# Kernel tuning notes

Measured on AMD Instinct MI355X. Metric: run time of the kernel, lower is better.

## Reference

```python
import jax, jax.numpy as jnp
import numpy as np
import math

NUM_EMBED = 1024
EMBED_FEATS = 256
IN_FEATS = 512
COMMITMENT_COST = 0.25
B, T = 16, 4096


def setup_inputs() -> dict:
    key = jax.random.key(0)
    k1, k2, k3, k4 = jax.random.split(key, 4)
    inputs = jax.random.normal(k1, (B, IN_FEATS, T), dtype=jnp.float32)
    # Conv1d(kernel_size=1) == per-position linear: weight [E, C_in], bias [E]
    proj_w = jax.random.normal(k2, (EMBED_FEATS, IN_FEATS), dtype=jnp.float32) / np.sqrt(IN_FEATS)
    proj_b = jax.random.normal(k3, (EMBED_FEATS,), dtype=jnp.float32) * 0.01
    embed = jax.random.normal(k4, (NUM_EMBED, EMBED_FEATS), dtype=jnp.float32)
    return {"inputs": inputs, "proj_w": proj_w, "proj_b": proj_b, "embed": embed}


def reference(inputs, proj_w, proj_b, embed):
    sg = jax.lax.stop_gradient
    b, c_in, t = inputs.shape
    # 1x1 conv projection then transpose(1,-1): [B, T, E]
    x = jnp.einsum('bct,ec->bte', inputs, proj_w) + proj_b
    flat = x.reshape(-1, EMBED_FEATS)  # [B*T, E]
    d2 = (jnp.sum(flat * flat, axis=1, keepdims=True)
          + jnp.sum(embed * embed, axis=1)
          - 2.0 * flat @ embed.T)  # [B*T, num_embed]
    q_idx = jnp.argmin(d2, axis=1)  # [B*T]
    # one-hot @ embed == direct gather (same math, same gradient structure)
    z_q = embed[q_idx].reshape(x.shape)  # [B, T, E]
    vq_loss = jnp.mean((z_q - sg(x)) ** 2)
    commitment_loss = jnp.mean((sg(z_q) - x) ** 2)
    loss = vq_loss + COMMITMENT_COST * commitment_loss
    z_q_st = x + sg(z_q - x)  # straight-through
    n_tokens = flat.shape[0]
    probs = jnp.zeros((NUM_EMBED,), dtype=jnp.float32).at[q_idx].add(1.0) / n_tokens
    log_perplexity = -jnp.sum(probs * jnp.log(probs + 1e-10))
    num_spatial = n_tokens / b
    kldiv_r = math.log(NUM_EMBED) * num_spatial * jnp.ones((b, 1), dtype=jnp.float32)
    z_q_out = jnp.swapaxes(z_q_st, 1, 2)  # [B, E, T]
    return z_q_out, loss, kldiv_r, log_perplexity
```

## Files before the change

kernel.cpp:

```cpp
#include <hip/hip_runtime.h>
#include <hip/hip_bf16.h>
#include <math.h>

#define TT   4096
#define BB   16
#define NTOK 65536
#define CIN  512
#define EF   256
#define NE   1024

typedef __attribute__((ext_vector_type(8))) short bf16x8;
typedef __attribute__((ext_vector_type(4))) float f32x4;

static __device__ __forceinline__ unsigned short f2bf(float f) {
  unsigned int u = __float_as_uint(f);
  u += 0x7fffu + ((u >> 16) & 1u);
  return (unsigned short)(u >> 16);
}

#define GLL(gsrc, ldst) \
  __builtin_amdgcn_global_load_lds((const __attribute__((address_space(1))) void*)(gsrc), \
                                   (__attribute__((address_space(3))) void*)(ldst), 16, 0, 0)

__global__ __launch_bounds__(256) void k_prep(const float* __restrict__ Wf,
                                              const float* __restrict__ Ef,
                                              unsigned short* __restrict__ Wbf,
                                              unsigned short* __restrict__ Ebf,
                                              float* __restrict__ e_norm) {
  int bid = blockIdx.x;
  if (bid < 512) {
    int i = bid * 256 + threadIdx.x;
    Wbf[i] = f2bf(Wf[i]);
  } else if (bid < 1536) {
    int i = (bid - 512) * 256 + threadIdx.x;
    Ebf[i] = f2bf(-2.0f * Ef[i]);
  } else {
    int w = threadIdx.x >> 6, l = threadIdx.x & 63;
    int k = (bid - 1536) * 4 + w;
    const float4 v4 = ((const float4*)(Ef + (size_t)k * EF))[l];
    float s = v4.x * v4.x + v4.y * v4.y + v4.z * v4.z + v4.w * v4.w;
    for (int off = 32; off; off >>= 1) s += __shfl_down(s, off);
    if (l == 0) e_norm[k] = s;
  }
}

__global__ __launch_bounds__(256, 2) void k_gemm1(const float* __restrict__ in,
                                                  const unsigned short* __restrict__ Wbf,
                                                  const float* __restrict__ bias,
                                                  unsigned short* __restrict__ x_bf,
                                                  float* __restrict__ sse) {
  __shared__ unsigned short lds[20480];
  unsigned short* as_ = lds;
  unsigned short* bs  = lds + 4096;
  unsigned short* xs  = lds;

  int tid = threadIdx.x;
  int w = tid >> 6, l = tid & 63;
  int l15 = l & 15, quad = l >> 4;
  int tok0 = blockIdx.x * 64;
  const float* src = in + (size_t)(tok0 >> 12) * CIN * TT + (tok0 & 4095);

  f32x4 acc[4][4];
#pragma unroll
  for (int a = 0; a < 4; ++a)
#pragma unroll
    for (int b = 0; b < 4; ++b) acc[a][b] = (f32x4){0.f, 0.f, 0.f, 0.f};

  float v[16];
  {
    const float* s0 = src + (size_t)(w * 16) * TT + l;
#pragma unroll
    for (int i = 0; i < 16; ++i) v[i] = s0[(size_t)i * TT];
  }
  for (int ks = 0; ks < 8; ++ks) {
    int k0 = ks * 64;
#pragma unroll
    for (int i = 0; i < 8; ++i) {
      int g = i * 256 + tid;
      int row = g >> 3, pc = g & 7, lc = pc ^ (row & 7);
      GLL(Wbf + (size_t)row * CIN + k0 + lc * 8, bs + g * 8);
    }
#pragma unroll
    for (int cc = 0; cc < 2; ++cc) {
      alignas(16) unsigned short tmp[8];
#pragma unroll
      for (int j = 0; j < 8; ++j) tmp[j] = f2bf(v[cc * 8 + j]);
      int c8 = w * 2 + cc;
      int pc = c8 ^ (l & 7);
      *(bf16x8*)(as_ + l * 64 + pc * 8) = *(const bf16x8*)tmp;
    }
    __syncthreads();
    if (ks < 7) {
      const float* s0 = src + (size_t)(k0 + 64 + w * 16) * TT + l;
#pragma unroll
      for (int i = 0; i < 16; ++i) v[i] = s0[(size_t)i * TT];
    }
#pragma unroll
    for (int kstep = 0; kstep < 2; ++kstep) {
      int ck = kstep * 4 + quad;
      bf16x8 af[4], bfr[4];
#pragma unroll
      for (int msub = 0; msub < 4; ++msub) {
        int row = msub * 16 + l15;
        int pa = ck ^ (row & 7);
        af[msub] = *(const bf16x8*)(as_ + row * 64 + pa * 8);
      }
#pragma unroll
      for (int nsub = 0; nsub < 4; ++nsub) {
        int row = w * 64 + nsub * 16 + l15;
        int pb = ck ^ (row & 7);
        bfr[nsub] = *(const bf16x8*)(bs + row * 64 + pb * 8);
      }
#pragma unroll
      for (int msub = 0; msub < 4; ++msub)
#pragma unroll
        for (int nsub = 0; nsub < 4; ++nsub)
          acc[msub][nsub] = __builtin_amdgcn_mfma_f32_16x16x32_bf16(af[msub], bfr[nsub],
                                                                    acc[msub][nsub], 0, 0, 0);
    }
    __syncthreads();
  }

  float xsq = 0.f;
#pragma unroll
  for (int nsub = 0; nsub < 4; ++nsub) {
    int e = w * 64 + nsub * 16 + l15;
    float bv = bias[e];
    int cx = e >> 3;
#pragma unroll
    for (int msub = 0; msub < 4; ++msub)
#pragma unroll
      for (int reg = 0; reg < 4; ++reg) {
        int m = msub * 16 + quad * 4 + reg;
        float x = acc[msub][nsub][reg] + bv;
        xsq += x * x;
        int pcx = cx ^ (m & 31);
        xs[m * 256 + pcx * 8 + (e & 7)] = f2bf(x);
      }
  }
  __syncthreads();
#pragma unroll
  for (int i = 0; i < 8; ++i) {
    int g = i * 256 + tid;
    int m = g >> 5, c = g & 31;
    int pcx = c ^ (m & 31);
    bf16x8 val = *(const bf16x8*)(xs + m * 256 + pcx * 8);
    *(bf16x8*)(x_bf + (size_t)(tok0 + m) * EF + c * 8) = val;
  }
  __shared__ float xred[4];
  for (int off = 32; off; off >>= 1) xsq += __shfl_down(xsq, off);
  if (l == 0) xred[w] = xsq;
  __syncthreads();
  if (tid == 0) atomicAdd(sse, xred[0] + xred[1] + xred[2] + xred[3]);
}

__global__ __launch_bounds__(256, 1) void k_dist(const unsigned short* __restrict__ x_bf,
                                                 const unsigned short* __restrict__ Ebf,
                                                 const float* __restrict__ e_norm,
                                                 const float* __restrict__ embed,
                                                 float* __restrict__ out,
                                                 unsigned int* __restrict__ hist,
                                                 float* __restrict__ sse) {
  __shared__ unsigned short lds[32768];
  float* zq    = (float*)lds;
  int* idxs    = (int*)(lds + 30720);
  float* svred = (float*)(lds + 31488);

  int tid = threadIdx.x;
  int w = tid >> 6, l = tid & 63;
  int l15 = l & 15, quad = l >> 4;
  int tok0 = blockIdx.x * 128;

  bf16x8 af[2][8];
#pragma unroll
  for (int msub = 0; msub < 2; ++msub)
#pragma unroll
    for (int kst = 0; kst < 8; ++kst) {
      int row = tok0 + w * 32 + msub * 16 + l15;
      af[msub][kst] = *(const bf16x8*)(x_bf + (size_t)row * EF + (kst * 4 + quad) * 8);
    }

#pragma unroll
  for (int i = 0; i < 8; ++i) {
    int g = i * 256 + tid;
    int row = g >> 5, pcc = g & 31, lc = pcc ^ (row & 31);
    GLL(Ebf + (size_t)row * EF + lc * 8, lds + g * 8);
  }
  float enn[4];
#pragma unroll
  for (int nsub = 0; nsub < 4; ++nsub) enn[nsub] = e_norm[nsub * 16 + l15];
  __syncthreads();

  float best_v[2][4];
  int best_i[2][4];
#pragma unroll
  for (int a = 0; a < 2; ++a)
#pragma unroll
    for (int b = 0; b < 4; ++b) { best_v[a][b] = 3.0e38f; best_i[a][b] = 0; }

  for (int chunk = 0; chunk < 16; ++chunk) {
    int c0 = chunk * 64;
    unsigned short* eb = lds + (chunk & 1) * 16384;
    if (chunk < 15) {
      unsigned short* ebn = lds + ((chunk & 1) ^ 1) * 16384;
#pragma unroll
      for (int i = 0; i < 8; ++i) {
        int g = i * 256 + tid;
        int row = g >> 5, pcc = g & 31, lc = pcc ^ (row & 31);
        GLL(Ebf + (size_t)(c0 + 64 + row) * EF + lc * 8, ebn + g * 8);
      }
    }
    f32x4 dacc[2][4];
#pragma unroll
    for (int nsub = 0; nsub < 4; ++nsub) {
      float en = enn[nsub];
      dacc[0][nsub] = (f32x4){en, en, en, en};
      dacc[1][nsub] = (f32x4){en, en, en, en};
    }
    if (chunk < 15) {
#pragma unroll
      for (int nsub = 0; nsub < 4; ++nsub) enn[nsub] = e_norm[c0 + 64 + nsub * 16 + l15];
    }
#pragma unroll
    for (int nsub = 0; nsub < 4; ++nsub) {
      int n = nsub * 16 + l15;
#pragma unroll
      for (int kst = 0; kst < 8; ++kst) {
        int pc = (kst * 4 + quad) ^ (n & 31);
        bf16x8 bfr = *(const bf16x8*)(eb + n * 256 + pc * 8);
        dacc[0][nsub] = __builtin_amdgcn_mfma_f32_16x16x32_bf16(af[0][kst], bfr,
                                                                dacc[0][nsub], 0, 0, 0);
        dacc[1][nsub] = __builtin_amdgcn_mfma_f32_16x16x32_bf16(af[1][kst], bfr,
                                                                dacc[1][nsub], 0, 0, 0);
      }
    }
#pragma unroll
    for (int msub = 0; msub < 2; ++msub)
#pragma unroll
      for (int nsub = 0; nsub < 4; ++nsub) {
        int code = c0 + nsub * 16 + l15;
#pragma unroll
        for (int reg = 0; reg < 4; ++reg) {
          float vv = dacc[msub][nsub][reg];
          if (vv < best_v[msub][reg]) { best_v[msub][reg] = vv; best_i[msub][reg] = code; }
        }
      }
    __syncthreads();
  }

  float sv = 0.f;
#pragma unroll
  for (int msub = 0; msub < 2; ++msub)
#pragma unroll
    for (int reg = 0; reg < 4; ++reg) {
      float vv = best_v[msub][reg];
      int idx = best_i[msub][reg];
#pragma unroll
      for (int off = 8; off; off >>= 1) {
        float ov = __shfl_xor(vv, off, 16);
        int oi = __shfl_xor(idx, off, 16);
        if (ov < vv || (ov == vv && oi < idx)) { vv = ov; idx = oi; }
      }
      if (l15 == 0) {
        int m = w * 32 + msub * 16 + quad * 4 + reg;
        idxs[m] = idx;
        atomicAdd(&hist[idx], 1u);
        sv += vv;
      }
    }
  for (int off = 32; off; off >>= 1) sv += __shfl_down(sv, off);
  if (l == 0) svred[w] = sv;
  __syncthreads();
  if (tid == 0) atomicAdd(sse, svred[0] + svred[1] + svred[2] + svred[3]);

  int b = tok0 >> 12, t0 = tok0 & 4095;
  int tg = tid >> 4;
  for (int pass = 0; pass < 4; ++pass) {
    int e0 = pass * 64;
    __syncthreads();
    for (int r = 0; r < 8; ++r) {
      int tl = r * 16 + tg;
      const float4 vv = *(const float4*)(embed + (size_t)idxs[tl] * EF + e0 + l15 * 4);
      float* zr = zq + tl * 65 + l15 * 4;
      zr[0] = vv.x; zr[1] = vv.y; zr[2] = vv.z; zr[3] = vv.w;
    }
    __syncthreads();
    int tl4 = (tid & 31) * 4;
    for (int r = 0; r < 8; ++r) {
      int e = r * 8 + (tid >> 5);
      float4 vv;
      vv.x = zq[(tl4 + 0) * 65 + e];
      vv.y = zq[(tl4 + 1) * 65 + e];
      vv.z = zq[(tl4 + 2) * 65 + e];
      vv.w = zq[(tl4 + 3) * 65 + e];
      *(float4*)(out + ((size_t)(b * EF + e0 + e) << 12) + t0 + tl4) = vv;
    }
  }
}

__global__ __launch_bounds__(256) void k_final(const unsigned int* __restrict__ hist,
                                               const float* __restrict__ sse,
                                               float* __restrict__ out) {
  __shared__ float red[4];
  int tid = threadIdx.x;
  float local = 0.f;
  for (int i = tid; i < NE; i += 256) {
    float p = (float)hist[i] * (1.0f / 65536.0f);
    local -= p * logf(p + 1e-10f);
  }
  for (int off = 32; off; off >>= 1) local += __shfl_down(local, off);
  if ((tid & 63) == 0) red[tid >> 6] = local;
  __syncthreads();
  if (tid == 0) {
    float lp = red[0] + red[1] + red[2] + red[3];
    out[16777216] = 1.25f * sse[0] / 16777216.0f;
    out[16777233] = lp;
  }
  if (tid < 16) out[16777217 + tid] = 6.93147180559945f * 4096.0f;
}

extern "C" void kernel_launch(void* const* d_in, const int* in_sizes, int n_in,
                              void* d_out, int out_size, void* d_ws, size_t ws_size,
                              hipStream_t stream) {
  const float* inputs = (const float*)d_in[0];
  const float* proj_w = (const float*)d_in[1];
  const float* proj_b = (const float*)d_in[2];
  const float* embed = (const float*)d_in[3];
  float* out = (float*)d_out;
  char* ws = (char*)d_ws;

  unsigned short* x_bf = (unsigned short*)(ws);
  unsigned short* Wbf  = (unsigned short*)(ws + 33554432);
  unsigned short* Ebf  = (unsigned short*)(ws + 33816576);
  float* e_norm        = (float*)(ws + 34340864);
  unsigned int* hist   = (unsigned int*)(ws + 34344960);
  float* sse           = (float*)(ws + 34349056);
  if (ws_size < 34349060) return;

  hipMemsetAsync(ws + 34344960, 0, 4100, stream);

  k_prep<<<1792, 256, 0, stream>>>(proj_w, embed, Wbf, Ebf, e_norm);
  k_gemm1<<<1024, 256, 0, stream>>>(inputs, Wbf, proj_b, x_bf, sse);
  k_dist<<<512, 256, 0, stream>>>(x_bf, Ebf, e_norm, embed, out, hist, sse);
  k_final<<<1, 256, 0, stream>>>(hist, sse, out);
}
```

Before: 306.9 us.

## Widen GEMM and distance kernels to 512 threads, split codebook across wave halves

Result: slower. 654.8 us (+113.3%).

```diff
diff --git a/kernel.cpp b/kernel.cpp
--- a/kernel.cpp
+++ b/kernel.cpp
@@ -28,36 +28,41 @@
                                               unsigned short* __restrict__ Ebf,
                                               float* __restrict__ e_norm) {
   int bid = blockIdx.x;
-  if (bid < 512) {
-    int i = bid * 256 + threadIdx.x;
-    Wbf[i] = f2bf(Wf[i]);
-  } else if (bid < 1536) {
-    int i = (bid - 512) * 256 + threadIdx.x;
-    Ebf[i] = f2bf(-2.0f * Ef[i]);
+  int tid = threadIdx.x;
+  if (bid < 128) {
+    int i = bid * 256 + tid;
+    float4 v = ((const float4*)Wf)[i];
+    ushort4 o = {f2bf(v.x), f2bf(v.y), f2bf(v.z), f2bf(v.w)};
+    ((ushort4*)Wbf)[i] = o;
   } else {
-    int w = threadIdx.x >> 6, l = threadIdx.x & 63;
-    int k = (bid - 1536) * 4 + w;
-    const float4 v4 = ((const float4*)(Ef + (size_t)k * EF))[l];
-    float s = v4.x * v4.x + v4.y * v4.y + v4.z * v4.z + v4.w * v4.w;
+    int eb = bid - 128;
+    int i = eb * 256 + tid;
+    float4 v = ((const float4*)Ef)[i];
+    float s = v.x * v.x + v.y * v.y + v.z * v.z + v.w * v.w;
+    ushort4 o = {f2bf(-2.f * v.x), f2bf(-2.f * v.y), f2bf(-2.f * v.z), f2bf(-2.f * v.w)};
+    ((ushort4*)Ebf)[i] = o;
+    int w = tid >> 6, l = tid & 63;
     for (int off = 32; off; off >>= 1) s += __shfl_down(s, off);
-    if (l == 0) e_norm[k] = s;
-  }
-}
-
-__global__ __launch_bounds__(256, 2) void k_gemm1(const float* __restrict__ in,
+    if (l == 0) e_norm[eb * 4 + w] = s;
+  }
+}
+
+__global__ __launch_bounds__(512, 2) void k_gemm1(const float* __restrict__ in,
                                                   const unsigned short* __restrict__ Wbf,
                                                   const float* __restrict__ bias,
                                                   unsigned short* __restrict__ x_bf,
                                                   float* __restrict__ sse) {
-  __shared__ unsigned short lds[20480];
-  unsigned short* as_ = lds;
-  unsigned short* bs  = lds + 4096;
+  __shared__ unsigned short lds[40960];
+  float* af32 = (float*)lds;
+  unsigned short* as_ = lds + 16384;
+  unsigned short* bs  = lds + 24576;
   unsigned short* xs  = lds;
 
   int tid = threadIdx.x;
   int w = tid >> 6, l = tid & 63;
   int l15 = l & 15, quad = l >> 4;
-  int tok0 = blockIdx.x * 64;
+  int tq = w & 1, eq = w >> 1;
+  int tok0 = blockIdx.x * 128;
   const float* src = in + (size_t)(tok0 >> 12) * CIN * TT + (tok0 & 4095);
 
   f32x4 acc[4][4];
@@ -66,48 +71,49 @@
 #pragma unroll
     for (int b = 0; b < 4; ++b) acc[a][b] = (f32x4){0.f, 0.f, 0.f, 0.f};
 
-  float v[16];
-  {
-    const float* s0 = src + (size_t)(w * 16) * TT + l;
-#pragma unroll
-    for (int i = 0; i < 16; ++i) v[i] = s0[(size_t)i * TT];
-  }
+  int tconv = tid & 127, cg = tid >> 7;
+
   for (int ks = 0; ks < 8; ++ks) {
     int k0 = ks * 64;
 #pragma unroll
-    for (int i = 0; i < 8; ++i) {
-      int g = i * 256 + tid;
+    for (int i = 0; i < 4; ++i) {
+      int g = i * 512 + tid;
       int row = g >> 3, pc = g & 7, lc = pc ^ (row & 7);
       GLL(Wbf + (size_t)row * CIN + k0 + lc * 8, bs + g * 8);
     }
 #pragma unroll
+    for (int i = 0; i < 4; ++i) {
+      int g = i * 512 + tid;
+      int c = g >> 5, col = g & 31;
+      GLL(src + (size_t)(k0 + c) * TT + col * 4, ((unsigned short*)af32) + g * 8);
+    }
+    __syncthreads();
+    float vv[16];
+#pragma unroll
+    for (int i = 0; i < 16; ++i) vv[i] = af32[(cg * 16 + i) * 128 + tconv];
+#pragma unroll
     for (int cc = 0; cc < 2; ++cc) {
       alignas(16) unsigned short tmp[8];
 #pragma unroll
-      for (int j = 0; j < 8; ++j) tmp[j] = f2bf(v[cc * 8 + j]);
-      int c8 = w * 2 + cc;
-      int pc = c8 ^ (l & 7);
-      *(bf16x8*)(as_ + l * 64 + pc * 8) = *(const bf16x8*)tmp;
-    }
-    __syncthreads();
-    if (ks < 7) {
-      const float* s0 = src + (size_t)(k0 + 64 + w * 16) * TT + l;
-#pragma unroll
-      for (int i = 0; i < 16; ++i) v[i] = s0[(size_t)i * TT];
-    }
+      for (int j = 0; j < 8; ++j) tmp[j] = f2bf(vv[cc * 8 + j]);
+      int c8 = cg * 2 + cc;
+      int pc = c8 ^ (tconv & 7);
+      *(bf16x8*)(as_ + tconv * 64 + pc * 8) = *(const bf16x8*)tmp;
+    }
+    __syncthreads();
 #pragma unroll
     for (int kstep = 0; kstep < 2; ++kstep) {
       int ck = kstep * 4 + quad;
       bf16x8 af[4], bfr[4];
 #pragma unroll
       for (int msub = 0; msub < 4; ++msub) {
-        int row = msub * 16 + l15;
+        int row = tq * 64 + msub * 16 + l15;
         int pa = ck ^ (row & 7);
         af[msub] = *(const bf16x8*)(as_ + row * 64 + pa * 8);
       }
 #pragma unroll
       for (int nsub = 0; nsub < 4; ++nsub) {
-        int row = w * 64 + nsub * 16 + l15;
+        int row = eq * 64 + nsub * 16 + l15;
         int pb = ck ^ (row & 7);
         bfr[nsub] = *(const bf16x8*)(bs + row * 64 + pb * 8);
       }
@@ -124,14 +130,14 @@
   float xsq = 0.f;
 #pragma unroll
   for (int nsub = 0; nsub < 4; ++nsub) {
-    int e = w * 64 + nsub * 16 + l15;
+    int e = eq * 64 + nsub * 16 + l15;
     float bv = bias[e];
     int cx = e >> 3;
 #pragma unroll
     for (int msub = 0; msub < 4; ++msub)
 #pragma unroll
       for (int reg = 0; reg < 4; ++reg) {
-        int m = msub * 16 + quad * 4 + reg;
+        int m = tq * 64 + msub * 16 + quad * 4 + reg;
         float x = acc[msub][nsub][reg] + bv;
         xsq += x * x;
         int pcx = cx ^ (m & 31);
@@ -140,21 +146,26 @@
   }
   __syncthreads();
 #pragma unroll
-  for (int i = 0; i < 8; ++i) {
-    int g = i * 256 + tid;
+  for (int i = 0; i < 4; ++i) {
+    int g = i * 512 + tid;
     int m = g >> 5, c = g & 31;
     int pcx = c ^ (m & 31);
     bf16x8 val = *(const bf16x8*)(xs + m * 256 + pcx * 8);
     *(bf16x8*)(x_bf + (size_t)(tok0 + m) * EF + c * 8) = val;
   }
-  __shared__ float xred[4];
+  __shared__ float xred[8];
   for (int off = 32; off; off >>= 1) xsq += __shfl_down(xsq, off);
   if (l == 0) xred[w] = xsq;
   __syncthreads();
-  if (tid == 0) atomicAdd(sse, xred[0] + xred[1] + xred[2] + xred[3]);
-}
-
-__global__ __launch_bounds__(256, 1) void k_dist(const unsigned short* __restrict__ x_bf,
+  if (tid == 0) {
+    float t = 0.f;
+#pragma unroll
+    for (int i = 0; i < 8; ++i) t += xred[i];
+    atomicAdd(sse, t);
+  }
+}
+
+__global__ __launch_bounds__(512, 2) void k_dist(const unsigned short* __restrict__ x_bf,
                                                  const unsigned short* __restrict__ Ebf,
                                                  const float* __restrict__ e_norm,
                                                  const float* __restrict__ embed,
@@ -162,13 +173,16 @@
                                                  unsigned int* __restrict__ hist,
                                                  float* __restrict__ sse) {
   __shared__ unsigned short lds[32768];
-  float* zq    = (float*)lds;
-  int* idxs    = (int*)(lds + 30720);
-  float* svred = (float*)(lds + 31488);
+  float* redv  = (float*)lds;
+  int*   redi  = (int*)lds + 256;
+  int*   idxs  = (int*)lds + 512;
+  float* svred = (float*)lds + 640;
+  float* zq    = (float*)lds + 1024;
 
   int tid = threadIdx.x;
   int w = tid >> 6, l = tid & 63;
   int l15 = l & 15, quad = l >> 4;
+  int g3 = w & 3, h = w >> 2;
   int tok0 = blockIdx.x * 128;
 
   bf16x8 af[2][8];
@@ -176,19 +190,21 @@
   for (int msub = 0; msub < 2; ++msub)
 #pragma unroll
     for (int kst = 0; kst < 8; ++kst) {
-      int row = tok0 + w * 32 + msub * 16 + l15;
+      int row = tok0 + g3 * 32 + msub * 16 + l15;
       af[msub][kst] = *(const bf16x8*)(x_bf + (size_t)row * EF + (kst * 4 + quad) * 8);
     }
 
 #pragma unroll
-  for (int i = 0; i < 8; ++i) {
-    int g = i * 256 + tid;
-    int row = g >> 5, pcc = g & 31, lc = pcc ^ (row & 31);
-    GLL(Ebf + (size_t)row * EF + lc * 8, lds + g * 8);
-  }
-  float enn[4];
-#pragma unroll
-  for (int nsub = 0; nsub < 4; ++nsub) enn[nsub] = e_norm[nsub * 16 + l15];
+  for (int i = 0; i < 4; ++i) {
+    int g = i * 512 + tid;
+    int half = g >> 10, gg = g & 1023;
+    int row = gg >> 5, pcc = gg & 31, lc = pcc ^ (row & 31);
+    GLL(Ebf + (size_t)(half * 512 + row) * EF + lc * 8,
+        lds + half * 16384 + gg * 8);
+  }
+  float enn[2];
+  enn[0] = e_norm[h * 512 + l15];
+  enn[1] = e_norm[h * 512 + 16 + l15];
   __syncthreads();
 
   float best_v[2][4];
@@ -199,34 +215,35 @@
     for (int b = 0; b < 4; ++b) { best_v[a][b] = 3.0e38f; best_i[a][b] = 0; }
 
   for (int chunk = 0; chunk < 16; ++chunk) {
-    int c0 = chunk * 64;
-    unsigned short* eb = lds + (chunk & 1) * 16384;
+    int par = chunk & 1;
     if (chunk < 15) {
-      unsigned short* ebn = lds + ((chunk & 1) ^ 1) * 16384;
-#pragma unroll
-      for (int i = 0; i < 8; ++i) {
-        int g = i * 256 + tid;
-        int row = g >> 5, pcc = g & 31, lc = pcc ^ (row & 31);
-        GLL(Ebf + (size_t)(c0 + 64 + row) * EF + lc * 8, ebn + g * 8);
-      }
-    }
-    f32x4 dacc[2][4];
-#pragma unroll
-    for (int nsub = 0; nsub < 4; ++nsub) {
+#pragma unroll
+      for (int i = 0; i < 4; ++i) {
+        int g = i * 512 + tid;
+        int half = g >> 10, gg = g & 1023;
+        int row = gg >> 5, pcc = gg & 31, lc = pcc ^ (row & 31);
+        GLL(Ebf + (size_t)(half * 512 + (chunk + 1) * 32 + row) * EF + lc * 8,
+            lds + half * 16384 + (par ^ 1) * 8192 + gg * 8);
+      }
+    }
+    const unsigned short* eb = lds + h * 16384 + par * 8192;
+    f32x4 dacc[2][2];
+#pragma unroll
+    for (int nsub = 0; nsub < 2; ++nsub) {
       float en = enn[nsub];
       dacc[0][nsub] = (f32x4){en, en, en, en};
       dacc[1][nsub] = (f32x4){en, en, en, en};
     }
     if (chunk < 15) {
-#pragma unroll
-      for (int nsub = 0; nsub < 4; ++nsub) enn[nsub] = e_norm[c0 + 64 + nsub * 16 + l15];
-    }
-#pragma unroll
-    for (int nsub = 0; nsub < 4; ++nsub) {
+      enn[0] = e_norm[h * 512 + (chunk + 1) * 32 + l15];
+      enn[1] = e_norm[h * 512 + (chunk + 1) * 32 + 16 + l15];
+    }
+#pragma unroll
+    for (int nsub = 0; nsub < 2; ++nsub) {
       int n = nsub * 16 + l15;
 #pragma unroll
       for (int kst = 0; kst < 8; ++kst) {
-        int pc = (kst * 4 + quad) ^ (n & 31);
+        int pc = (kst * 4 + quad) ^ n;
         bf16x8 bfr = *(const bf16x8*)(eb + n * 256 + pc * 8);
         dacc[0][nsub] = __builtin_amdgcn_mfma_f32_16x16x32_bf16(af[0][kst], bfr,
                                                                 dacc[0][nsub], 0, 0, 0);
@@ -237,8 +254,8 @@
 #pragma unroll
     for (int msub = 0; msub < 2; ++msub)
 #pragma unroll
-      for (int nsub = 0; nsub < 4; ++nsub) {
-        int code = c0 + nsub * 16 + l15;
+      for (int nsub = 0; nsub < 2; ++nsub) {
+        int code = h * 512 + chunk * 32 + nsub * 16 + l15;
 #pragma unroll
         for (int reg = 0; reg < 4; ++reg) {
           float vv = dacc[msub][nsub][reg];
@@ -248,7 +265,6 @@
     __syncthreads();
   }
 
-  float sv = 0.f;
 #pragma unroll
   for (int msub = 0; msub < 2; ++msub)
 #pragma unroll
@@ -262,38 +278,48 @@
         if (ov < vv || (ov == vv && oi < idx)) { vv = ov; idx = oi; }
       }
       if (l15 == 0) {
-        int m = w * 32 + msub * 16 + quad * 4 + reg;
-        idxs[m] = idx;
-        atomicAdd(&hist[idx], 1u);
-        sv += vv;
-      }
-    }
-  for (int off = 32; off; off >>= 1) sv += __shfl_down(sv, off);
-  if (l == 0) svred[w] = sv;
-  __syncthreads();
-  if (tid == 0) atomicAdd(sse, svred[0] + svred[1] + svred[2] + svred[3]);
+        int tokloc = g3 * 32 + msub * 16 + quad * 4 + reg;
+        redv[h * 128 + tokloc] = vv;
+        redi[h * 128 + tokloc] = idx;
+      }
+    }
+  __syncthreads();
+  if (tid < 128) {
+    float v0 = redv[tid], v1 = redv[128 + tid];
+    int i0 = redi[tid], i1 = redi[128 + tid];
+    float vv; int idx;
+    if (v1 < v0 || (v1 == v0 && i1 < i0)) { vv = v1; idx = i1; } else { vv = v0; idx = i0; }
+    idxs[tid] = idx;
+    atomicAdd(&hist[idx], 1u);
+    for (int off = 32; off; off >>= 1) vv += __shfl_down(vv, off);
+    if ((tid & 63) == 0) svred[tid >> 6] = vv;
+  }
+  __syncthreads();
+  if (tid == 0) atomicAdd(sse, svred[0] + svred[1]);
 
   int b = tok0 >> 12, t0 = tok0 & 4095;
-  int tg = tid >> 4;
   for (int pass = 0; pass < 4; ++pass) {
     int e0 = pass * 64;
-    __syncthreads();
-    for (int r = 0; r < 8; ++r) {
-      int tl = r * 16 + tg;
-      const float4 vv = *(const float4*)(embed + (size_t)idxs[tl] * EF + e0 + l15 * 4);
-      float* zr = zq + tl * 65 + l15 * 4;
+    if (pass) __syncthreads();
+    for (int r = 0; r < 4; ++r) {
+      int tl = r * 32 + (tid >> 4);
+      const float4 vv = *(const float4*)(embed + (size_t)idxs[tl] * EF + e0 + (tid & 15) * 4);
+      float* zr = zq + tl * 65 + (tid & 15) * 4;
       zr[0] = vv.x; zr[1] = vv.y; zr[2] = vv.z; zr[3] = vv.w;
     }
     __syncthreads();
-    int tl4 = (tid & 31) * 4;
-    for (int r = 0; r < 8; ++r) {
-      int e = r * 8 + (tid >> 5);
-      float4 vv;
-      vv.x = zq[(tl4 + 0) * 65 + e];
-      vv.y = zq[(tl4 + 1) * 65 + e];
-      vv.z = zq[(tl4 + 2) * 65 + e];
-      vv.w = zq[(tl4 + 3) * 65 + e];
-      *(float4*)(out + ((size_t)(b * EF + e0 + e) << 12) + t0 + tl4) = vv;
+    int e = tid >> 3, sub = tid & 7;
+#pragma unroll
+    for (int j = 0; j < 2; ++j) {
+      int t4 = sub * 16 + j * 8;
+      float4 va, vb;
+      va.x = zq[(t4 + 0) * 65 + e]; va.y = zq[(t4 + 1) * 65 + e];
+      va.z = zq[(t4 + 2) * 65 + e]; va.w = zq[(t4 + 3) * 65 + e];
+      vb.x = zq[(t4 + 4) * 65 + e]; vb.y = zq[(t4 + 5) * 65 + e];
+      vb.z = zq[(t4 + 6) * 65 + e]; vb.w = zq[(t4 + 7) * 65 + e];
+      float* op = out + ((size_t)(b * EF + e0 + e) << 12) + t0 + t4;
+      *(float4*)op = va;
+      *(float4*)(op + 4) = vb;
     }
   }
 }
@@ -339,8 +365,8 @@
 
   hipMemsetAsync(ws + 34344960, 0, 4100, stream);
 
-  k_prep<<<1792, 256, 0, stream>>>(proj_w, embed, Wbf, Ebf, e_norm);
-  k_gemm1<<<1024, 256, 0, stream>>>(inputs, Wbf, proj_b, x_bf, sse);
-  k_dist<<<512, 256, 0, stream>>>(x_bf, Ebf, e_norm, embed, out, hist, sse);
+  k_prep<<<384, 256, 0, stream>>>(proj_w, embed, Wbf, Ebf, e_norm);
+  k_gemm1<<<512, 512, 0, stream>>>(inputs, Wbf, proj_b, x_bf, sse);
+  k_dist<<<512, 512, 0, stream>>>(x_bf, Ebf, e_norm, embed, out, hist, sse);
   k_final<<<1, 256, 0, stream>>>(hist, sse, out);
 }
```
